# Performance work log

Measured on AMD Instinct MI355X. Metric: run time of the kernel, lower is better.

The kernel has to match this reference:

```python
import jax, jax.numpy as jnp
import numpy as np

N = 20000       # nodes
C = 64          # channels per irrep
E = 320000      # edges (avg degree 16)
S = 64          # num_species
R = 8           # radial embedding dim
HR = 64         # radial MLP hidden
HEADS = 2       # readout heads
AVG = 16.0      # avg_num_neighbors
SOFT = 2.0      # soft_normalization


def setup_inputs() -> dict:
    key = jax.random.key(0)
    ks = jax.random.split(key, 28)
    g = lambda k, sh, sc=1.0: jax.random.normal(k, sh, dtype=jnp.float32) * sc
    inv = lambda n: 1.0 / float(np.sqrt(n))
    return {
        "edge_vectors": g(ks[0], (E, 3)),
        "node_feats_s": g(ks[1], (N, C)),
        "node_feats_v": g(ks[2], (N, C, 3)),
        "radial_embeddings": g(ks[3], (E, R)),
        "node_species": jax.random.randint(ks[4], (N,), 0, S),
        "senders": jax.random.randint(ks[5], (E,), 0, N),
        "receivers": jax.random.randint(ks[6], (E,), 0, N),
        # residual FullyConnectedTensorProduct(feats, one-hot species) weights
        "W_rs": g(ks[7], (S, C, C), inv(C)),
        "W_rv": g(ks[8], (S, C, C), inv(C)),
        # interaction: linear up, radial MLP (5 TP paths), linear down
        "W_up_s": g(ks[9], (C, C), inv(C)),
        "W_up_v": g(ks[10], (C, C), inv(C)),
        "Wr1": g(ks[11], (R, HR), inv(R)),
        "Wr2": g(ks[12], (HR, 5 * C), inv(HR)),
        "W_down_s": g(ks[13], (C, C), inv(C)),
        "W_down_v": g(ks[14], (C, C), inv(C)),
        # equivariant product basis: per-channel species-indexed symmetric-contraction weights
        "w1s": g(ks[15], (S, C)),
        "w1v": g(ks[16], (S, C)),
        "w2ss": g(ks[17], (S, C)),
        "w2vv": g(ks[18], (S, C)),
        "w2sv": g(ks[19], (S, C)),
        "W_prod_s": g(ks[20], (C, C), inv(C)),
        "W_prod_v": g(ks[21], (C, C), inv(C)),
        # linear readout heads (out_irreps -> 1x0e per head)
        "w_read": g(ks[22], (HEADS, C), inv(C)),
    }


def reference(edge_vectors, node_feats_s, node_feats_v, radial_embeddings,
              node_species, senders, receivers,
              W_rs, W_rv, W_up_s, W_up_v, Wr1, Wr2, W_down_s, W_down_v,
              w1s, w1v, w2ss, w2vv, w2sv, W_prod_s, W_prod_v, w_read):
    n_nodes = node_feats_s.shape[0]
    sp = node_species

    # --- residual connection: FCTP(feats, one-hot(species)) == species-indexed channel mix
    res_s = jnp.einsum('nc,ncd->nd', node_feats_s, W_rs[sp])
    res_v = jnp.einsum('ncx,ncd->ndx', node_feats_v, W_rv[sp])

    # --- InteractionBlock ---
    s_u = node_feats_s @ W_up_s
    v_u = jnp.einsum('ncx,cd->ndx', node_feats_v, W_up_v)
    nrm = jnp.linalg.norm(edge_vectors, axis=-1, keepdims=True)
    u = edge_vectors / jnp.maximum(nrm, 1e-9)  # l=1 spherical harmonic direction [E,3]
    # radial MLP -> per-edge per-channel weights for the 5 CG paths of (0e+1o)x(0e+1o)->0e+1o
    w = (jax.nn.silu(radial_embeddings @ Wr1) @ Wr2).reshape(-1, 5, s_u.shape[1])
    se = s_u[senders]            # [E,C] gather (irregular)
    ve = v_u[senders]            # [E,C,3]
    dot = jnp.einsum('ecx,ex->ec', ve, u)          # 1o x 1o -> 0e
    crs = jnp.cross(ve, u[:, None, :])             # 1o x 1o -> 1o
    m_s = w[:, 0] * se + w[:, 3] * dot
    m_v = (w[:, 1][..., None] * ve
           + w[:, 2][..., None] * u[:, None, :]
           + w[:, 4][..., None] * crs)
    a_s = jax.ops.segment_sum(m_s, receivers, num_segments=n_nodes) / AVG
    a_v = jax.ops.segment_sum(m_v, receivers, num_segments=n_nodes) / AVG
    a_s = a_s @ W_down_s
    a_v = jnp.einsum('ncx,cd->ndx', a_v, W_down_v)

    # --- EquivariantProductBasisBlock: symmetric contraction (correlation<=2), per-channel
    # species-indexed weights, followed by a linear to out_irreps ---
    vv = jnp.sum(a_v * a_v, axis=-1)                                   # 1o (x) 1o -> 0e
    p_s = w1s[sp] * a_s + w2ss[sp] * a_s * a_s + w2vv[sp] * vv
    p_v = w1v[sp][..., None] * a_v + w2sv[sp][..., None] * a_s[..., None] * a_v
    p_s = p_s @ W_prod_s
    p_v = jnp.einsum('ncx,cd->ndx', p_v, W_prod_v)

    # --- soft normalization: phi(n) = 1/(1 + n*sus(n)), n = norm/SOFT ---
    def sus(x):
        return jnp.where(x > 0, jnp.exp(-1.0 / jnp.where(x > 0, x, 1.0)), 0.0)

    def phi(n):
        n = n / SOFT
        return 1.0 / (1.0 + n * sus(n))

    f_s = p_s * phi(jnp.abs(p_s))
    f_v = p_v * phi(jnp.linalg.norm(p_v, axis=-1, keepdims=True))

    # --- residual add ---
    f_s = f_s + res_s
    f_v = f_v + res_v

    # --- readout heads (Linear out_irreps -> 1x0e), stacked on axis=1 ---
    node_out = jnp.einsum('nc,hc->nh', f_s, w_read)
    return (node_out, f_s, f_v)
```

## Files before the change

### kernel.cpp

```cpp
#include <hip/hip_runtime.h>

#define N_NODES 20000
#define C 64
#define E_EDGES 320000
#define S_SPEC 64
#define R_DIM 8
#define HR 64
#define HEADS 2
#define TE 128
#define NT (E_EDGES/TE)
#define HPAD 68
#define INV_AVG (1.0f/16.0f)

#define FS_OFF 40000
#define FV_OFF 1320000

typedef short bf16x4 __attribute__((ext_vector_type(4)));
typedef float f32x4  __attribute__((ext_vector_type(4)));

__device__ __forceinline__ unsigned short f2bf(float f){
  unsigned u = __float_as_uint(f);
  u += 0x7fffu + ((u >> 16) & 1u);
  return (unsigned short)(u >> 16);
}
__device__ __forceinline__ float phi_f(float x){
  float n = x * 0.5f;
  float s = (n > 0.0f) ? expf(-1.0f/n) : 0.0f;
  return 1.0f / (1.0f + n * s);
}

__global__ __launch_bounds__(256) void wr2t_kernel(const float* __restrict__ Wr2,
                                                   unsigned short* __restrict__ wr2t){
  int idx = blockIdx.x*256 + threadIdx.x;
  int n = idx >> 6, k = idx & 63;
  wr2t[idx] = f2bf(Wr2[k*320 + n] * INV_AVG);
}

__global__ __launch_bounds__(256) void node_up_kernel(
    const float* __restrict__ fs, const float* __restrict__ fv,
    const float* __restrict__ Wus, const float* __restrict__ Wuv,
    float* __restrict__ s_u, float* __restrict__ v_u){
  const int ni = threadIdx.x >> 6;
  const int d  = threadIdx.x & 63;
  const int n  = blockIdx.x*4 + ni;
  __shared__ float s_l[4][C];
  __shared__ float v_l[4][3][C];
  s_l[ni][d] = fs[n*C + d];
  #pragma unroll
  for (int x = 0; x < 3; ++x) v_l[ni][x][d] = fv[(n*C + d)*3 + x];
  __syncthreads();
  float as = 0.f, a0 = 0.f, a1 = 0.f, a2 = 0.f;
  #pragma unroll 4
  for (int c = 0; c < C; ++c){
    float wsv = Wus[c*C + d];
    float wvv = Wuv[c*C + d];
    as += s_l[ni][c] * wsv;
    a0 += v_l[ni][0][c] * wvv;
    a1 += v_l[ni][1][c] * wvv;
    a2 += v_l[ni][2][c] * wvv;
  }
  s_u[n*C + d] = as;
  v_u[(n*3 + 0)*C + d] = a0;
  v_u[(n*3 + 1)*C + d] = a1;
  v_u[(n*3 + 2)*C + d] = a2;
}

__global__ __launch_bounds__(256) void hist_kernel(const int* __restrict__ rcv, int* __restrict__ count){
  int e = blockIdx.x*256 + threadIdx.x;
  atomicAdd(&count[rcv[e]], 1);
}

__global__ __launch_bounds__(1024) void scan_kernel(const int* __restrict__ count, int* __restrict__ cursor){
  __shared__ int sums[1024];
  const int t = threadIdx.x;
  const int base = t*20;
  int s = 0;
  #pragma unroll 4
  for (int i = 0; i < 20; ++i){ int idx = base+i; if (idx < N_NODES) s += count[idx]; }
  sums[t] = s;
  __syncthreads();
  for (int off = 1; off < 1024; off <<= 1){
    int v = (t >= off) ? sums[t-off] : 0;
    __syncthreads();
    sums[t] += v;
    __syncthreads();
  }
  int run = (t > 0) ? sums[t-1] : 0;
  for (int i = 0; i < 20; ++i){
    int idx = base+i;
    if (idx < N_NODES){ cursor[idx] = run; run += count[idx]; }
  }
}

__global__ __launch_bounds__(256) void scatter_kernel(
    const int* __restrict__ snd, const int* __restrict__ rcv,
    const float* __restrict__ ev, const float* __restrict__ re,
    int* __restrict__ cursor,
    int* __restrict__ snd_s, int* __restrict__ rcv_s,
    float* __restrict__ ev_s, float* __restrict__ re_s){
  int e = blockIdx.x*256 + threadIdx.x;
  int r = rcv[e];
  int pos = atomicAdd(&cursor[r], 1);
  snd_s[pos] = snd[e];
  rcv_s[pos] = r;
  ev_s[pos*3+0] = ev[e*3+0];
  ev_s[pos*3+1] = ev[e*3+1];
  ev_s[pos*3+2] = ev[e*3+2];
  const float4* rp = (const float4*)&re[(size_t)e*R_DIM];
  float4 ra = rp[0], rb = rp[1];
  float4* op = (float4*)&re_s[(size_t)pos*R_DIM];
  op[0] = ra; op[1] = rb;
}

__global__ __launch_bounds__(512, 4) void edge_kernel(
    const float* __restrict__ ev_s, const float* __restrict__ re_s,
    const int* __restrict__ snd_s, const int* __restrict__ rcv_s,
    const float* __restrict__ Wr1, const unsigned short* __restrict__ wr2t,
    const float* __restrict__ s_u, const float* __restrict__ v_u,
    float* __restrict__ a_s, float* __restrict__ a_v)
{
  __shared__ __align__(16) float Wr1_l[R_DIM*HR];
  __shared__ __align__(16) unsigned short Wr2T_l[320*HPAD];
  __shared__ __align__(16) unsigned short h_l[TE*HPAD];
  __shared__ float u_l[TE][4];
  __shared__ int snd_l[TE];
  __shared__ int rcv_l[TE];

  const int t = threadIdx.x;
  const int lane = t & 63;
  const int w = t >> 6;
  int b = blockIdx.x;
  int xcd = b & 7, idx = b >> 3;
  const int q = NT >> 3, r = NT & 7;
  int tile = (xcd < r ? xcd*(q+1) : r*(q+1) + (xcd-r)*q) + idx;
  const int e0 = tile * TE;

  Wr1_l[t] = Wr1[t];
  #pragma unroll
  for (int j = 0; j < 10; ++j){
    int i4 = t + 512*j;
    ushort4 v4 = ((const ushort4*)wr2t)[i4];
    int el = i4*4; int n = el >> 6, k = el & 63;
    *(ushort4*)&Wr2T_l[n*HPAD + k] = v4;
  }
  if (t < TE){
    int e = e0 + t;
    float x = ev_s[e*3+0], y = ev_s[e*3+1], z = ev_s[e*3+2];
    float nr = sqrtf(x*x + y*y + z*z);
    float inv = 1.0f / fmaxf(nr, 1e-9f);
    u_l[t][0] = x*inv; u_l[t][1] = y*inv; u_l[t][2] = z*inv;
    snd_l[t] = snd_s[e];
    rcv_l[t] = rcv_s[e];
  }
  __syncthreads();

  {
    int e = t & 127, qh = t >> 7;
    const float4* rp = (const float4*)&re_s[(size_t)(e0 + e)*R_DIM];
    float4 ra = rp[0], rb = rp[1];
    unsigned short hh[16];
    #pragma unroll
    for (int kk = 0; kk < 16; ++kk){
      int k = qh*16 + kk;
      float acc = ra.x*Wr1_l[0*HR+k] + ra.y*Wr1_l[1*HR+k] + ra.z*Wr1_l[2*HR+k] + ra.w*Wr1_l[3*HR+k]
                + rb.x*Wr1_l[4*HR+k] + rb.y*Wr1_l[5*HR+k] + rb.z*Wr1_l[6*HR+k] + rb.w*Wr1_l[7*HR+k];
      hh[kk] = f2bf(acc / (1.0f + expf(-acc)));
    }
    #pragma unroll
    for (int j4 = 0; j4 < 4; ++j4)
      *(ushort4*)&h_l[e*HPAD + qh*16 + j4*4] = *(ushort4*)&hh[j4*4];
  }
  __syncthreads();

  f32x4 acc[20];
  #pragma unroll
  for (int cf = 0; cf < 20; ++cf) acc[cf] = (f32x4){0.f,0.f,0.f,0.f};
  {
    const int arow = (w*16 + (lane & 15))*HPAD;
    const int koff = 4*(lane >> 4);
    #pragma unroll
    for (int kt = 0; kt < 4; ++kt){
      bf16x4 af = *(const bf16x4*)&h_l[arow + kt*16 + koff];
      #pragma unroll
      for (int cf = 0; cf < 20; ++cf){
        bf16x4 bf = *(const bf16x4*)&Wr2T_l[(cf*16 + (lane & 15))*HPAD + kt*16 + koff];
        acc[cf] = __builtin_amdgcn_mfma_f32_16x16x16bf16_1k(af, bf, acc[cf], 0, 0, 0);
      }
    }
  }

  {
    const int ebase = w*16 + (lane >> 4)*4;
    const int cl = lane & 15;
    float ms[4], mv0[4], mv1[4], mv2[4];
    #pragma unroll
    for (int k2 = 0; k2 < 4; ++k2){ ms[k2]=0.f; mv0[k2]=0.f; mv1[k2]=0.f; mv2[k2]=0.f; }
    int cur = rcv_l[ebase];
    #pragma unroll
    for (int i = 0; i < 4; ++i){
      int el = ebase + i;
      int rc = rcv_l[el];
      if (rc != cur){
        #pragma unroll
        for (int k2 = 0; k2 < 4; ++k2){
          int c = k2*16 + cl;
          unsafeAtomicAdd(&a_s[cur*C + c],       ms[k2]);
          unsafeAtomicAdd(&a_v[(cur*3+0)*C + c], mv0[k2]);
          unsafeAtomicAdd(&a_v[(cur*3+1)*C + c], mv1[k2]);
          unsafeAtomicAdd(&a_v[(cur*3+2)*C + c], mv2[k2]);
          ms[k2]=0.f; mv0[k2]=0.f; mv1[k2]=0.f; mv2[k2]=0.f;
        }
        cur = rc;
      }
      int sn = snd_l[el];
      float u0 = u_l[el][0], u1 = u_l[el][1], u2 = u_l[el][2];
      const float* sp_ = &s_u[sn*C];
      const float* vp_ = &v_u[sn*3*C];
      #pragma unroll
      for (int k2 = 0; k2 < 4; ++k2){
        int c = k2*16 + cl;
        float se  = sp_[c];
        float ve0 = vp_[c];
        float ve1 = vp_[C + c];
        float ve2 = vp_[2*C + c];
        float w0 = acc[0*4+k2][i];
        float w1 = acc[1*4+k2][i];
        float w2 = acc[2*4+k2][i];
        float w3 = acc[3*4+k2][i];
        float w4 = acc[4*4+k2][i];
        float dt  = ve0*u0 + ve1*u1 + ve2*u2;
        float cr0 = ve1*u2 - ve2*u1;
        float cr1 = ve2*u0 - ve0*u2;
        float cr2 = ve0*u1 - ve1*u0;
        ms[k2]  += w0*se + w3*dt;
        mv0[k2] += w1*ve0 + w2*u0 + w4*cr0;
        mv1[k2] += w1*ve1 + w2*u1 + w4*cr1;
        mv2[k2] += w1*ve2 + w2*u2 + w4*cr2;
      }
    }
    #pragma unroll
    for (int k2 = 0; k2 < 4; ++k2){
      int c = k2*16 + cl;
      unsafeAtomicAdd(&a_s[cur*C + c],       ms[k2]);
      unsafeAtomicAdd(&a_v[(cur*3+0)*C + c], mv0[k2]);
      unsafeAtomicAdd(&a_v[(cur*3+1)*C + c], mv1[k2]);
      unsafeAtomicAdd(&a_v[(cur*3+2)*C + c], mv2[k2]);
    }
  }
}

__global__ __launch_bounds__(256) void node_post_kernel(
    const float* __restrict__ a_s, const float* __restrict__ a_v,
    const float* __restrict__ fs_in, const float* __restrict__ fv_in,
    const int* __restrict__ species,
    const float* __restrict__ W_rs, const float* __restrict__ W_rv,
    const float* __restrict__ W_ds, const float* __restrict__ W_dv,
    const float* __restrict__ w1s, const float* __restrict__ w1v,
    const float* __restrict__ w2ss, const float* __restrict__ w2vv, const float* __restrict__ w2sv,
    const float* __restrict__ W_ps, const float* __restrict__ W_pv,
    const float* __restrict__ w_read, float* __restrict__ out)
{
  const int ni = threadIdx.x >> 6;
  const int d  = threadIdx.x & 63;
  const int n  = blockIdx.x*4 + ni;
  const int sp = species[n];
  __shared__ float as_l[4][C];
  __shared__ float av_l[4][3][C];
  __shared__ float si_l[4][C];
  __shared__ float vi_l[4][3][C];
  as_l[ni][d] = a_s[n*C + d];
  #pragma unroll
  for (int x=0;x<3;x++) av_l[ni][x][d] = a_v[(n*3+x)*C + d];
  si_l[ni][d] = fs_in[n*C + d];
  #pragma unroll
  for (int x=0;x<3;x++) vi_l[ni][x][d] = fv_in[(n*C + d)*3 + x];
  __syncthreads();
  const float* Wrs_p = W_rs + sp*C*C;
  const float* Wrv_p = W_rv + sp*C*C;
  float bs=0, bv0=0, bv1=0, bv2=0, rs=0, rv0=0, rv1=0, rv2=0;
  for (int c=0;c<C;++c){
    float wds = W_ds[c*C+d], wdv = W_dv[c*C+d];
    float wrs = Wrs_p[c*C+d], wrv = Wrv_p[c*C+d];
    bs  += as_l[ni][c]*wds;
    bv0 += av_l[ni][0][c]*wdv; bv1 += av_l[ni][1][c]*wdv; bv2 += av_l[ni][2][c]*wdv;
    rs  += si_l[ni][c]*wrs;
    rv0 += vi_l[ni][0][c]*wrv; rv1 += vi_l[ni][1][c]*wrv; rv2 += vi_l[ni][2][c]*wrv;
  }
  float vv = bv0*bv0 + bv1*bv1 + bv2*bv2;
  float ps  = w1s[sp*C+d]*bs + w2ss[sp*C+d]*bs*bs + w2vv[sp*C+d]*vv;
  float c1v = w1v[sp*C+d], c2sv = w2sv[sp*C+d];
  float pv0 = c1v*bv0 + c2sv*bs*bv0;
  float pv1 = c1v*bv1 + c2sv*bs*bv1;
  float pv2 = c1v*bv2 + c2sv*bs*bv2;
  __syncthreads();
  as_l[ni][d] = ps; av_l[ni][0][d]=pv0; av_l[ni][1][d]=pv1; av_l[ni][2][d]=pv2;
  __syncthreads();
  float qs=0, qv0=0, qv1=0, qv2=0;
  for (int c=0;c<C;++c){
    float wps = W_ps[c*C+d], wpv = W_pv[c*C+d];
    qs  += as_l[ni][c]*wps;
    qv0 += av_l[ni][0][c]*wpv; qv1 += av_l[ni][1][c]*wpv; qv2 += av_l[ni][2][c]*wpv;
  }
  float fsv = qs * phi_f(fabsf(qs)) + rs;
  float nv = sqrtf(qv0*qv0 + qv1*qv1 + qv2*qv2);
  float ph = phi_f(nv);
  float fv0 = qv0*ph + rv0;
  float fv1 = qv1*ph + rv1;
  float fv2 = qv2*ph + rv2;
  out[FS_OFF + n*C + d] = fsv;
  float* fvo = &out[FV_OFF + (size_t)(n*C + d)*3];
  fvo[0]=fv0; fvo[1]=fv1; fvo[2]=fv2;
  #pragma unroll
  for (int h=0; h<HEADS; ++h){
    float r = fsv * w_read[h*C + d];
    #pragma unroll
    for (int off=32; off>0; off>>=1) r += __shfl_down(r, off);
    if (d == 0) out[n*HEADS + h] = r;
  }
}

extern "C" void kernel_launch(void* const* d_in, const int* in_sizes, int n_in,
                              void* d_out, int out_size, void* d_ws, size_t ws_size,
                              hipStream_t stream)
{
  const float* ev   = (const float*)d_in[0];
  const float* nfs  = (const float*)d_in[1];
  const float* nfv  = (const float*)d_in[2];
  const float* re   = (const float*)d_in[3];
  const int*   spec = (const int*)d_in[4];
  const int*   snd  = (const int*)d_in[5];
  const int*   rcv  = (const int*)d_in[6];
  const float* W_rs = (const float*)d_in[7];
  const float* W_rv = (const float*)d_in[8];
  const float* Wus  = (const float*)d_in[9];
  const float* Wuv  = (const float*)d_in[10];
  const float* Wr1  = (const float*)d_in[11];
  const float* Wr2  = (const float*)d_in[12];
  const float* Wds  = (const float*)d_in[13];
  const float* Wdv  = (const float*)d_in[14];
  const float* w1s  = (const float*)d_in[15];
  const float* w1v  = (const float*)d_in[16];
  const float* w2ss = (const float*)d_in[17];
  const float* w2vv = (const float*)d_in[18];
  const float* w2sv = (const float*)d_in[19];
  const float* Wps  = (const float*)d_in[20];
  const float* Wpv  = (const float*)d_in[21];
  const float* wrd  = (const float*)d_in[22];

  float* out = (float*)d_out;
  float* ws  = (float*)d_ws;
  float* s_u   = ws;
  float* v_u   = ws +  1280000;
  float* a_s   = ws +  5120000;
  float* a_v   = ws +  6400000;
  int*   count = (int*)(ws + 10240000);
  int*   cursr = (int*)(ws + 10260000);
  int*   snd_s = (int*)(ws + 10280000);
  int*   rcv_s = (int*)(ws + 10600000);
  float* ev_s  = ws + 10920000;
  float* re_s  = ws + 11880000;
  unsigned short* wr2t = (unsigned short*)(ws + 14440000);

  hipMemsetAsync(a_s, 0, (size_t)5120000*sizeof(float), stream);
  hipMemsetAsync(count, 0, (size_t)N_NODES*sizeof(int), stream);

  wr2t_kernel<<<(320*64)/256, 256, 0, stream>>>(Wr2, wr2t);
  node_up_kernel<<<N_NODES/4, 256, 0, stream>>>(nfs, nfv, Wus, Wuv, s_u, v_u);
  hist_kernel<<<E_EDGES/256, 256, 0, stream>>>(rcv, count);
  scan_kernel<<<1, 1024, 0, stream>>>(count, cursr);
  scatter_kernel<<<E_EDGES/256, 256, 0, stream>>>(snd, rcv, ev, re, cursr,
                                                  snd_s, rcv_s, ev_s, re_s);
  edge_kernel<<<NT, 512, 0, stream>>>(ev_s, re_s, snd_s, rcv_s, Wr1, wr2t,
                                      s_u, v_u, a_s, a_v);
  node_post_kernel<<<N_NODES/4, 256, 0, stream>>>(a_s, a_v, nfs, nfv, spec,
      W_rs, W_rv, Wds, Wdv, w1s, w1v, w2ss, w2vv, w2sv, Wps, Wpv, wrd, out);
}
```

Before: 420.4 us.

## Pack node-up features as bf16 and gather edges through a permutation index

Node-up outputs are packed into one interleaved bf16 ushort4 per node-channel, so each sender gather becomes a single 8-byte load instead of four separate fp32 loads. The scatter kernel that copied sorted edge data is replaced by a permutation kernel, and the edge kernel reads the original edge arrays through that permutation. Sender gathers are also hoisted ahead of the radial MLP so they can overlap with compute. This cuts gather traffic and a full copy pass, at the cost of bf16 rounding in messages and uncoalesced indirect edge reads.

Result: slower. 451.5 us (+7.4%).

```diff
diff --git a/kernel.cpp b/kernel.cpp
--- a/kernel.cpp
+++ b/kernel.cpp
@@ -23,6 +23,9 @@
   u += 0x7fffu + ((u >> 16) & 1u);
   return (unsigned short)(u >> 16);
 }
+__device__ __forceinline__ float bf2f(unsigned short b){
+  return __uint_as_float(((unsigned)b) << 16);
+}
 __device__ __forceinline__ float phi_f(float x){
   float n = x * 0.5f;
   float s = (n > 0.0f) ? expf(-1.0f/n) : 0.0f;
@@ -39,7 +42,7 @@
 __global__ __launch_bounds__(256) void node_up_kernel(
     const float* __restrict__ fs, const float* __restrict__ fv,
     const float* __restrict__ Wus, const float* __restrict__ Wuv,
-    float* __restrict__ s_u, float* __restrict__ v_u){
+    ushort4* __restrict__ suv){
   const int ni = threadIdx.x >> 6;
   const int d  = threadIdx.x & 63;
   const int n  = blockIdx.x*4 + ni;
@@ -59,10 +62,9 @@
     a1 += v_l[ni][1][c] * wvv;
     a2 += v_l[ni][2][c] * wvv;
   }
-  s_u[n*C + d] = as;
-  v_u[(n*3 + 0)*C + d] = a0;
-  v_u[(n*3 + 1)*C + d] = a1;
-  v_u[(n*3 + 2)*C + d] = a2;
+  ushort4 o;
+  o.x = f2bf(as); o.y = f2bf(a0); o.z = f2bf(a1); o.w = f2bf(a2);
+  suv[(size_t)n*C + d] = o;
 }
 
 __global__ __launch_bounds__(256) void hist_kernel(const int* __restrict__ rcv, int* __restrict__ count){
@@ -92,31 +94,19 @@
   }
 }
 
-__global__ __launch_bounds__(256) void scatter_kernel(
+__global__ __launch_bounds__(256) void perm_kernel(
+    const int* __restrict__ rcv, int* __restrict__ cursor, int* __restrict__ perm){
+  int e = blockIdx.x*256 + threadIdx.x;
+  int pos = atomicAdd(&cursor[rcv[e]], 1);
+  perm[pos] = e;
+}
+
+__global__ __launch_bounds__(512, 4) void edge_kernel(
+    const float* __restrict__ ev, const float* __restrict__ re,
     const int* __restrict__ snd, const int* __restrict__ rcv,
-    const float* __restrict__ ev, const float* __restrict__ re,
-    int* __restrict__ cursor,
-    int* __restrict__ snd_s, int* __restrict__ rcv_s,
-    float* __restrict__ ev_s, float* __restrict__ re_s){
-  int e = blockIdx.x*256 + threadIdx.x;
-  int r = rcv[e];
-  int pos = atomicAdd(&cursor[r], 1);
-  snd_s[pos] = snd[e];
-  rcv_s[pos] = r;
-  ev_s[pos*3+0] = ev[e*3+0];
-  ev_s[pos*3+1] = ev[e*3+1];
-  ev_s[pos*3+2] = ev[e*3+2];
-  const float4* rp = (const float4*)&re[(size_t)e*R_DIM];
-  float4 ra = rp[0], rb = rp[1];
-  float4* op = (float4*)&re_s[(size_t)pos*R_DIM];
-  op[0] = ra; op[1] = rb;
-}
-
-__global__ __launch_bounds__(512, 4) void edge_kernel(
-    const float* __restrict__ ev_s, const float* __restrict__ re_s,
-    const int* __restrict__ snd_s, const int* __restrict__ rcv_s,
+    const int* __restrict__ perm,
     const float* __restrict__ Wr1, const unsigned short* __restrict__ wr2t,
-    const float* __restrict__ s_u, const float* __restrict__ v_u,
+    const ushort4* __restrict__ suv,
     float* __restrict__ a_s, float* __restrict__ a_v)
 {
   __shared__ __align__(16) float Wr1_l[R_DIM*HR];
@@ -125,6 +115,7 @@
   __shared__ float u_l[TE][4];
   __shared__ int snd_l[TE];
   __shared__ int rcv_l[TE];
+  __shared__ int pe_l[TE];
 
   const int t = threadIdx.x;
   const int lane = t & 63;
@@ -144,19 +135,30 @@
     *(ushort4*)&Wr2T_l[n*HPAD + k] = v4;
   }
   if (t < TE){
-    int e = e0 + t;
-    float x = ev_s[e*3+0], y = ev_s[e*3+1], z = ev_s[e*3+2];
+    int e = perm[e0 + t];
+    pe_l[t] = e;
+    float x = ev[e*3+0], y = ev[e*3+1], z = ev[e*3+2];
     float nr = sqrtf(x*x + y*y + z*z);
     float inv = 1.0f / fmaxf(nr, 1e-9f);
     u_l[t][0] = x*inv; u_l[t][1] = y*inv; u_l[t][2] = z*inv;
-    snd_l[t] = snd_s[e];
-    rcv_l[t] = rcv_s[e];
-  }
-  __syncthreads();
+    snd_l[t] = snd[e];
+    rcv_l[t] = rcv[e];
+  }
+  __syncthreads();
+
+  const int cl = lane & 15;
+  const int ebase = w*16 + (lane >> 4)*4;
+  ushort4 gv[4][4];
+  #pragma unroll
+  for (int i = 0; i < 4; ++i){
+    const ushort4* sp_ = &suv[(size_t)snd_l[ebase + i]*C];
+    #pragma unroll
+    for (int k2 = 0; k2 < 4; ++k2) gv[i][k2] = sp_[k2*16 + cl];
+  }
 
   {
     int e = t & 127, qh = t >> 7;
-    const float4* rp = (const float4*)&re_s[(size_t)(e0 + e)*R_DIM];
+    const float4* rp = (const float4*)&re[(size_t)pe_l[e]*R_DIM];
     float4 ra = rp[0], rb = rp[1];
     unsigned short hh[16];
     #pragma unroll
@@ -190,8 +192,6 @@
   }
 
   {
-    const int ebase = w*16 + (lane >> 4)*4;
-    const int cl = lane & 15;
     float ms[4], mv0[4], mv1[4], mv2[4];
     #pragma unroll
     for (int k2 = 0; k2 < 4; ++k2){ ms[k2]=0.f; mv0[k2]=0.f; mv1[k2]=0.f; mv2[k2]=0.f; }
@@ -212,17 +212,13 @@
         }
         cur = rc;
       }
-      int sn = snd_l[el];
       float u0 = u_l[el][0], u1 = u_l[el][1], u2 = u_l[el][2];
-      const float* sp_ = &s_u[sn*C];
-      const float* vp_ = &v_u[sn*3*C];
       #pragma unroll
       for (int k2 = 0; k2 < 4; ++k2){
-        int c = k2*16 + cl;
-        float se  = sp_[c];
-        float ve0 = vp_[c];
-        float ve1 = vp_[C + c];
-        float ve2 = vp_[2*C + c];
+        float se  = bf2f(gv[i][k2].x);
+        float ve0 = bf2f(gv[i][k2].y);
+        float ve1 = bf2f(gv[i][k2].z);
+        float ve2 = bf2f(gv[i][k2].w);
         float w0 = acc[0*4+k2][i];
         float w1 = acc[1*4+k2][i];
         float w2 = acc[2*4+k2][i];
@@ -349,29 +345,24 @@
 
   float* out = (float*)d_out;
   float* ws  = (float*)d_ws;
-  float* s_u   = ws;
-  float* v_u   = ws +  1280000;
-  float* a_s   = ws +  5120000;
-  float* a_v   = ws +  6400000;
-  int*   count = (int*)(ws + 10240000);
-  int*   cursr = (int*)(ws + 10260000);
-  int*   snd_s = (int*)(ws + 10280000);
-  int*   rcv_s = (int*)(ws + 10600000);
-  float* ev_s  = ws + 10920000;
-  float* re_s  = ws + 11880000;
-  unsigned short* wr2t = (unsigned short*)(ws + 14440000);
+  ushort4* suv  = (ushort4*)ws;
+  float*   a_s  = ws + 2560000;
+  float*   a_v  = ws + 3840000;
+  int*    count = (int*)(ws + 7680000);
+  int*    cursr = (int*)(ws + 7700000);
+  int*    perm  = (int*)(ws + 7720000);
+  unsigned short* wr2t = (unsigned short*)(ws + 8040000);
 
   hipMemsetAsync(a_s, 0, (size_t)5120000*sizeof(float), stream);
   hipMemsetAsync(count, 0, (size_t)N_NODES*sizeof(int), stream);
 
   wr2t_kernel<<<(320*64)/256, 256, 0, stream>>>(Wr2, wr2t);
-  node_up_kernel<<<N_NODES/4, 256, 0, stream>>>(nfs, nfv, Wus, Wuv, s_u, v_u);
+  node_up_kernel<<<N_NODES/4, 256, 0, stream>>>(nfs, nfv, Wus, Wuv, suv);
   hist_kernel<<<E_EDGES/256, 256, 0, stream>>>(rcv, count);
   scan_kernel<<<1, 1024, 0, stream>>>(count, cursr);
-  scatter_kernel<<<E_EDGES/256, 256, 0, stream>>>(snd, rcv, ev, re, cursr,
-                                                  snd_s, rcv_s, ev_s, re_s);
-  edge_kernel<<<NT, 512, 0, stream>>>(ev_s, re_s, snd_s, rcv_s, Wr1, wr2t,
-                                      s_u, v_u, a_s, a_v);
+  perm_kernel<<<E_EDGES/256, 256, 0, stream>>>(rcv, cursr, perm);
+  edge_kernel<<<NT, 512, 0, stream>>>(ev, re, snd, rcv, perm, Wr1, wr2t,
+                                      suv, a_s, a_v);
   node_post_kernel<<<N_NODES/4, 256, 0, stream>>>(a_s, a_v, nfs, nfv, spec,
       W_rs, W_rv, Wds, Wdv, w1s, w1v, w2ss, w2vv, w2sv, Wps, Wpv, wrd, out);
 }
```
